# Kernel tuning notes

Hardware: AMD Instinct MI355X
Metric: run time of the kernel (lower is better)

Reference implementation:

```python
import jax, jax.numpy as jnp
import numpy as np

BEAM = 64
RANK = 32
VOCAB = 21128


def setup_inputs() -> dict:
    key = jax.random.key(0)
    k1, k2, k3, k4 = jax.random.split(key, 4)
    B, S, V = 16, 256, VOCAB
    emissions = jax.random.normal(k1, (B, S, V), jnp.float32)
    targets = jax.random.randint(k2, (B, S), 0, V)
    mask = jnp.ones((B, S), dtype=bool)
    E1 = jax.random.normal(k3, (V, RANK), jnp.float32) * 0.02
    E2 = jax.random.normal(k4, (V, RANK), jnp.float32) * 0.02
    return {"emissions": emissions, "targets": targets, "mask": mask, "E1": E1, "E2": E2}


def _crf_llh(emissions, targets, mask, E1, E2, beam=BEAM):
    B, S, V = emissions.shape
    maskf = mask.astype(emissions.dtype)

    # ---- numerator: score of the target path ----
    em = jnp.take_along_axis(emissions, targets[:, :, None], axis=2)[:, :, 0]  # [B,S]
    trans = jnp.sum(E1[targets[:, :-1]] * E2[targets[:, 1:]], axis=2)          # [B,S-1]
    scores = em.at[:, 1:].add(trans)
    numerator = jnp.sum(scores * maskf, axis=1)                                # [B]

    # ---- denominator: beam-approximated normalizer ----
    # force target token into the beam (scatter +inf, then topk indices)
    b_idx = jnp.arange(B)[:, None]
    s_idx = jnp.arange(S)[None, :]
    _em = emissions.at[b_idx, s_idx, targets].set(jnp.inf)
    _, beam_targets = jax.lax.top_k(_em, beam)                                 # [B,S,beam]
    beam_em = jnp.take_along_axis(emissions, beam_targets, axis=2)             # [B,S,beam]

    t1 = E1[beam_targets[:, :-1]]                                              # [B,S-1,beam,rank]
    t2 = E2[beam_targets[:, 1:]]                                               # [B,S-1,beam,rank]
    beam_trans = jnp.einsum('bsir,bsjr->bsij', t1, t2)                         # [B,S-1,beam,beam]

    score0 = beam_em[:, 0]                                                     # [B,beam]

    def step(score, x):
        trans_i, emit_i, m_i = x
        nxt = jax.scipy.special.logsumexp(score[:, :, None] + trans_i, axis=1) + emit_i
        score = jnp.where(m_i[:, None], nxt, score)
        return score, None

    xs = (jnp.swapaxes(beam_trans, 0, 1),          # [S-1,B,beam,beam]
          jnp.swapaxes(beam_em[:, 1:], 0, 1),      # [S-1,B,beam]
          jnp.swapaxes(mask[:, 1:], 0, 1))         # [S-1,B]
    score, _ = jax.lax.scan(step, score0, xs)
    denominator = jax.scipy.special.logsumexp(score, axis=1)                   # [B]

    llh = numerator - denominator
    return jnp.sum(llh)  # reduction='sum'


def reference(emissions, targets, mask, E1, E2):
    return _crf_llh(emissions, targets, mask, E1, E2)
```

## Files before the change

### kernel.cpp

```cpp
#include <hip/hip_runtime.h>
#include <stdint.h>

#define Bn 16
#define Sn 256
#define Vn 21128
#define NV4 5282
#define RANKn 32
#define BEAMn 64
#define HBINS 4096
#define CAPn 512
#define NSEG 16
#define LOG2E 1.44269504088896340736f
#define LN2   0.69314718055994530942f

#define EXP2F(x) __builtin_amdgcn_exp2f(x)
#define LOG2F(x) __builtin_amdgcn_logf(x)

__device__ __forceinline__ unsigned f2o(unsigned b) {
    return (b & 0x80000000u) ? ~b : (b | 0x80000000u);
}
__device__ __forceinline__ float o2f(unsigned u) {
    unsigned b = (u & 0x80000000u) ? (u ^ 0x80000000u) : ~u;
    return __uint_as_float(b);
}
__device__ __forceinline__ float dot4(float4 a, float4 b) {
    return a.x * b.x + a.y * b.y + a.z * b.z + a.w * b.w;
}

__global__ __launch_bounds__(256) void topk_kernel(const float* __restrict__ emis,
                                                   const int* __restrict__ targets,
                                                   const int* __restrict__ mask,
                                                   const float* __restrict__ E1,
                                                   const float* __restrict__ E2,
                                                   int* __restrict__ beam_idx,
                                                   float* __restrict__ beam_val,
                                                   float* __restrict__ out) {
    const int row = blockIdx.x;
    const float* __restrict__ rowp = emis + (size_t)row * Vn;
    const int tgt = targets[row];
    __shared__ unsigned hist[HBINS];
    __shared__ unsigned csum[256];
    __shared__ unsigned cu[CAPn];
    __shared__ int      cix[CAPn];
    __shared__ int      selidx[BEAMn];
    __shared__ float    selval[BEAMn];
    __shared__ unsigned ccount;
    __shared__ int      binstar;
    __shared__ int      chunkc;
    __shared__ int      hastgt;
    __shared__ unsigned wcnt[4];
    const int t = threadIdx.x;
    if (t == 0) { ccount = 0; hastgt = 0; }

    const unsigned THRU = f2o(__float_as_uint(2.5f));
    uint4 vals[21];
    unsigned cntl = 0;
    #pragma unroll
    for (int it = 0; it < 21; ++it) {
        int v4 = t + it * 256;
        if (v4 < NV4) {
            const uint4 raw = ((const uint4*)rowp)[v4];
            uint4 u;
            u.x = f2o(raw.x); u.y = f2o(raw.y); u.z = f2o(raw.z); u.w = f2o(raw.w);
            vals[it] = u;
            cntl += (u.x > THRU) + (u.y > THRU) + (u.z > THRU) + (u.w > THRU);
        }
    }
    for (int off = 32; off; off >>= 1) cntl += __shfl_xor(cntl, off, 64);
    if ((t & 63) == 0) wcnt[t >> 6] = cntl;
    __syncthreads();
    const unsigned C0 = wcnt[0] + wcnt[1] + wcnt[2] + wcnt[3];

    if (C0 >= BEAMn && C0 <= CAPn) {
        #pragma unroll
        for (int it = 0; it < 21; ++it) {
            int v4 = t + it * 256;
            if (v4 < NV4) {
                uint4 u = vals[it];
                int bi = v4 * 4;
                if (u.x > THRU) { unsigned p = atomicAdd(&ccount, 1u); cu[p] = u.x; cix[p] = bi;     }
                if (u.y > THRU) { unsigned p = atomicAdd(&ccount, 1u); cu[p] = u.y; cix[p] = bi + 1; }
                if (u.z > THRU) { unsigned p = atomicAdd(&ccount, 1u); cu[p] = u.z; cix[p] = bi + 2; }
                if (u.w > THRU) { unsigned p = atomicAdd(&ccount, 1u); cu[p] = u.w; cix[p] = bi + 3; }
            }
        }
    } else {
        for (int i = t; i < HBINS; i += 256) hist[i] = 0;
        __syncthreads();
        #pragma unroll
        for (int it = 0; it < 21; ++it) {
            int v4 = t + it * 256;
            if (v4 < NV4) {
                uint4 u = vals[it];
                atomicAdd(&hist[u.x >> 20], 1u);
                atomicAdd(&hist[u.y >> 20], 1u);
                atomicAdd(&hist[u.z >> 20], 1u);
                atomicAdd(&hist[u.w >> 20], 1u);
            }
        }
        __syncthreads();
        unsigned cs = 0;
        #pragma unroll
        for (int i = 0; i < 16; ++i) cs += hist[t * 16 + i];
        csum[t] = cs;
        __syncthreads();
        for (int off = 1; off < 256; off <<= 1) {
            unsigned v = csum[t] + ((t + off < 256) ? csum[t + off] : 0u);
            __syncthreads();
            csum[t] = v;
            __syncthreads();
        }
        if (csum[t] >= BEAMn && (t == 255 || csum[t + 1] < BEAMn)) chunkc = t;
        __syncthreads();
        if (t == 0) {
            int tc = chunkc;
            unsigned acc = (tc == 255) ? 0u : csum[tc + 1];
            int bs = tc * 16;
            for (int b2 = tc * 16 + 15; b2 >= tc * 16; --b2) {
                acc += hist[b2];
                if (acc >= BEAMn) { bs = b2; break; }
            }
            binstar = bs;
        }
        __syncthreads();
        const unsigned bstar = (unsigned)binstar;
        #pragma unroll
        for (int it = 0; it < 21; ++it) {
            int v4 = t + it * 256;
            if (v4 < NV4) {
                uint4 u = vals[it];
                int bi = v4 * 4;
                if ((u.x >> 20) >= bstar) { unsigned p = atomicAdd(&ccount, 1u); if (p < CAPn) { cu[p] = u.x; cix[p] = bi;     } }
                if ((u.y >> 20) >= bstar) { unsigned p = atomicAdd(&ccount, 1u); if (p < CAPn) { cu[p] = u.y; cix[p] = bi + 1; } }
                if ((u.z >> 20) >= bstar) { unsigned p = atomicAdd(&ccount, 1u); if (p < CAPn) { cu[p] = u.z; cix[p] = bi + 2; } }
                if ((u.w >> 20) >= bstar) { unsigned p = atomicAdd(&ccount, 1u); if (p < CAPn) { cu[p] = u.w; cix[p] = bi + 3; } }
            }
        }
    }
    __syncthreads();
    const int C = (int)min(ccount, (unsigned)CAPn);
    for (int p = t; p < C; p += 256) {
        unsigned up = cu[p]; int ip = cix[p];
        int rank = 0;
        for (int q = 0; q < C; ++q) {
            unsigned uq = cu[q];
            rank += (uq > up) || (uq == up && cix[q] < ip);
        }
        if (rank < BEAMn) { selidx[rank] = ip; selval[rank] = o2f(up); }
    }
    __syncthreads();
    if (t < BEAMn && selidx[t] == tgt) hastgt = 1;
    __syncthreads();
    if (t == 0 && !hastgt) { selidx[BEAMn - 1] = tgt; selval[BEAMn - 1] = rowp[tgt]; }
    __syncthreads();
    if (t < BEAMn) {
        beam_idx[(size_t)row * BEAMn + t] = selidx[t];
        beam_val[(size_t)row * BEAMn + t] = selval[t];
    }
    if (t == 0) {
        const int s = row & (Sn - 1);
        float val = 0.f;
        if (mask[row]) {
            float em = rowp[tgt];
            float tr = 0.f;
            if (s > 0) {
                int pv = targets[row - 1];
                const float4* p1 = (const float4*)(E1 + (size_t)pv * RANKn);
                const float4* p2 = (const float4*)(E2 + (size_t)tgt * RANKn);
                #pragma unroll
                for (int r = 0; r < 8; ++r) tr += dot4(p1[r], p2[r]);
            }
            val = em + tr;
        }
        atomicAdd(out, val);
    }
}

#define TPAD 68
__global__ __launch_bounds__(256) void segprod_kernel(const float* __restrict__ E1,
                                                      const float* __restrict__ E2,
                                                      const int* __restrict__ beam_idx,
                                                      const float* __restrict__ beam_val,
                                                      const int* __restrict__ mask,
                                                      float* __restrict__ segP,
                                                      float* __restrict__ segL) {
    const int blk = blockIdx.x;
    const int b = blk >> 4, s = blk & 15;
    const int k0 = s * 16;
    const int nk = min(16, (Sn - 1) - k0);
    const float* __restrict__ bv  = beam_val + (size_t)b * Sn * BEAMn;
    const int* __restrict__ mk   = mask + (size_t)b * Sn;
    const int* __restrict__ bidx = beam_idx + (size_t)b * Sn * BEAMn;
    __shared__ float Qa[64][64], Qb[64][64];
    __shared__ float Mld[64][68];
    __shared__ float e1t[RANKn][TPAD];
    __shared__ float e2t[RANKn][TPAD];
    __shared__ float elog[16][64];
    __shared__ int   mvec[16];
    __shared__ float wmax[4];
    const int t = threadIdx.x;
    const int ti = t & 15, tj = t >> 4;
    const int i0 = ti * 4, j0 = tj * 4;

    for (int x = t; x < 4096; x += 256)
        (&Qa[0][0])[x] = ((x >> 6) == (x & 63)) ? 1.f : 0.f;
    for (int x = t; x < nk * 64; x += 256)
        elog[x >> 6][x & 63] = bv[(size_t)(k0 + (x >> 6) + 1) * BEAMn + (x & 63)] * LOG2E;
    if (t < nk) mvec[t] = mk[k0 + t + 1];
    __syncthreads();

    float (*Qc)[64] = Qa, (*Qn)[64] = Qb;
    float L = 0.f;
    const int srow = t >> 2, sq = t & 3;
    for (int kk = 0; kk < nk; ++kk) {
        const int live = mvec[kk];
        if (live) {
            const int rb = sq * 8;
            int i1 = bidx[(size_t)(k0 + kk) * BEAMn + srow];
            const float4* s1 = (const float4*)(E1 + (size_t)i1 * RANKn) + sq * 2;
            float4 a0 = s1[0], a1 = s1[1];
            int i2 = bidx[(size_t)(k0 + kk + 1) * BEAMn + srow];
            const float4* s2 = (const float4*)(E2 + (size_t)i2 * RANKn) + sq * 2;
            float4 b0 = s2[0], b1 = s2[1];
            e1t[rb + 0][srow] = a0.x; e1t[rb + 1][srow] = a0.y; e1t[rb + 2][srow] = a0.z; e1t[rb + 3][srow] = a0.w;
            e1t[rb + 4][srow] = a1.x; e1t[rb + 5][srow] = a1.y; e1t[rb + 6][srow] = a1.z; e1t[rb + 7][srow] = a1.w;
            e2t[rb + 0][srow] = b0.x; e2t[rb + 1][srow] = b0.y; e2t[rb + 2][srow] = b0.z; e2t[rb + 3][srow] = b0.w;
            e2t[rb + 4][srow] = b1.x; e2t[rb + 5][srow] = b1.y; e2t[rb + 6][srow] = b1.z; e2t[rb + 7][srow] = b1.w;
        }
        __syncthreads();
        if (live) {
            float macc[4][4] = {};
            #pragma unroll
            for (int r = 0; r < RANKn; ++r) {
                float4 a  = *(const float4*)&e1t[r][i0];
                float4 bb = *(const float4*)&e2t[r][j0];
                macc[0][0] += a.x * bb.x; macc[0][1] += a.x * bb.y; macc[0][2] += a.x * bb.z; macc[0][3] += a.x * bb.w;
                macc[1][0] += a.y * bb.x; macc[1][1] += a.y * bb.y; macc[1][2] += a.y * bb.z; macc[1][3] += a.y * bb.w;
                macc[2][0] += a.z * bb.x; macc[2][1] += a.z * bb.y; macc[2][2] += a.z * bb.z; macc[2][3] += a.z * bb.w;
                macc[3][0] += a.w * bb.x; macc[3][1] += a.w * bb.y; macc[3][2] += a.w * bb.z; macc[3][3] += a.w * bb.w;
            }
            const float4 el = *(const float4*)&elog[kk][j0];
            #pragma unroll
            for (int ii = 0; ii < 4; ++ii) {
                float4 o = { EXP2F(macc[ii][0] * LOG2E + el.x), EXP2F(macc[ii][1] * LOG2E + el.y),
                             EXP2F(macc[ii][2] * LOG2E + el.z), EXP2F(macc[ii][3] * LOG2E + el.w) };
                *(float4*)&Mld[i0 + ii][j0] = o;
            }
        }
        __syncthreads();
        float acc[4][4];
        if (live) {
            #pragma unroll
            for (int ii = 0; ii < 4; ++ii)
                #pragma unroll
                for (int jj = 0; jj < 4; ++jj) acc[ii][jj] = 0.f;
            for (int r = 0; r < 64; ++r) {
                float4 a  = *(const float4*)&Qc[r][i0];
                float4 bb = *(const float4*)&Mld[r][j0];
                acc[0][0] += a.x * bb.x; acc[0][1] += a.x * bb.y; acc[0][2] += a.x * bb.z; acc[0][3] += a.x * bb.w;
                acc[1][0] += a.y * bb.x; acc[1][1] += a.y * bb.y; acc[1][2] += a.y * bb.z; acc[1][3] += a.y * bb.w;
                acc[2][0] += a.z * bb.x; acc[2][1] += a.z * bb.y; acc[2][2] += a.z * bb.z; acc[2][3] += a.z * bb.w;
                acc[3][0] += a.w * bb.x; acc[3][1] += a.w * bb.y; acc[3][2] += a.w * bb.z; acc[3][3] += a.w * bb.w;
            }
            float lm = acc[0][0];
            #pragma unroll
            for (int ii = 0; ii < 4; ++ii)
                #pragma unroll
                for (int jj = 0; jj < 4; ++jj) lm = fmaxf(lm, acc[ii][jj]);
            for (int off = 32; off; off >>= 1) lm = fmaxf(lm, __shfl_xor(lm, off, 64));
            if ((t & 63) == 0) wmax[t >> 6] = lm;
        }
        __syncthreads();
        if (live) {
            const float m = fmaxf(fmaxf(wmax[0], wmax[1]), fmaxf(wmax[2], wmax[3]));
            const float inv = 1.f / m;
            #pragma unroll
            for (int jj = 0; jj < 4; ++jj) {
                float4 w = { acc[0][jj] * inv, acc[1][jj] * inv, acc[2][jj] * inv, acc[3][jj] * inv };
                *(float4*)&Qn[j0 + jj][i0] = w;
            }
            L += LOG2F(m);
            float (*tmp)[64] = Qc; Qc = Qn; Qn = tmp;
        }
        __syncthreads();
    }
    float* op = segP + (size_t)blk * 4096;
    for (int x = t; x < 4096; x += 256) op[x] = (&Qc[0][0])[x];
    if (t == 0) segL[blk] = L;
}

__global__ __launch_bounds__(256) void finale_kernel(const float* __restrict__ segP,
                                                     const float* __restrict__ segL,
                                                     const float* __restrict__ beam_val,
                                                     float* __restrict__ out) {
    const int b = blockIdx.x;
    const int t = threadIdx.x;
    const int w = t >> 6, j = t & 63;
    const float* __restrict__ bv = beam_val + (size_t)b * Sn * BEAMn;
    __shared__ float us[BEAMn];
    __shared__ float part[4][BEAMn + 1];
    float sc = bv[j] * LOG2E;
    float mx = sc;
    for (int off = 32; off; off >>= 1) mx = fmaxf(mx, __shfl_xor(mx, off, 64));
    float u = EXP2F(sc - mx);
    float Ltot = mx;
    const float* p0 = segP + ((size_t)b * NSEG) * 4096 + (size_t)j * 64 + w * 16;
    float4 ra0 = ((const float4*)p0)[0], ra1 = ((const float4*)p0)[1],
           ra2 = ((const float4*)p0)[2], ra3 = ((const float4*)p0)[3];
    for (int s2 = 0; s2 < NSEG; ++s2) {
        float4 rb0, rb1, rb2, rb3;
        if (s2 + 1 < NSEG) {
            const float* pn = segP + ((size_t)b * NSEG + s2 + 1) * 4096 + (size_t)j * 64 + w * 16;
            rb0 = ((const float4*)pn)[0]; rb1 = ((const float4*)pn)[1];
            rb2 = ((const float4*)pn)[2]; rb3 = ((const float4*)pn)[3];
        }
        if (w == 0) us[j] = u;
        __syncthreads();
        const float4* uu = (const float4*)&us[w * 16];
        float a2 = dot4(ra0, uu[0]) + dot4(ra1, uu[1]) + dot4(ra2, uu[2]) + dot4(ra3, uu[3]);
        part[w][j] = a2;
        __syncthreads();
        float tot = part[0][j] + part[1][j] + part[2][j] + part[3][j];
        float m = tot;
        for (int off = 32; off; off >>= 1) m = fmaxf(m, __shfl_xor(m, off, 64));
        u = tot / m;
        Ltot += LOG2F(m) + segL[b * NSEG + s2];
        ra0 = rb0; ra1 = rb1; ra2 = rb2; ra3 = rb3;
    }
    if (t < BEAMn) {
        float e = u;
        for (int off = 32; off; off >>= 1) e += __shfl_xor(e, off, 64);
        if (t == 0) atomicAdd(out, -LN2 * (Ltot + LOG2F(e)));
    }
}

extern "C" void kernel_launch(void* const* d_in, const int* in_sizes, int n_in,
                              void* d_out, int out_size, void* d_ws, size_t ws_size,
                              hipStream_t stream) {
    const float* emis    = (const float*)d_in[0];
    const int*   targets = (const int*)d_in[1];
    const int*   mask    = (const int*)d_in[2];
    const float* E1      = (const float*)d_in[3];
    const float* E2      = (const float*)d_in[4];
    float* out = (float*)d_out;
    char* ws = (char*)d_ws;
    int*   beam_idx = (int*)ws;
    float* beam_val = (float*)(ws + (1 << 20));
    float* segP     = (float*)(ws + (2 << 20));
    float* segL     = (float*)(ws + (7 << 20));

    (void)hipMemsetAsync(out, 0, sizeof(float), stream);
    hipLaunchKernelGGL(topk_kernel, dim3(Bn * Sn), dim3(256), 0, stream,
                       emis, targets, mask, E1, E2, beam_idx, beam_val, out);
    hipLaunchKernelGGL(segprod_kernel, dim3(Bn * NSEG), dim3(256), 0, stream,
                       E1, E2, beam_idx, beam_val, mask, segP, segL);
    hipLaunchKernelGGL(finale_kernel, dim3(Bn), dim3(256), 0, stream,
                       segP, segL, beam_val, out);
}
```

Before: 583.0 us.

## Split beam recurrence into 32 shorter segments and normalize once per segment

The sequence is split into 32 segments of 8 steps instead of 16 segments of 16. This doubles the number of segment-product blocks and halves the serial chain each block walks. The per-step max reduction, its extra barrier and the rescale are removed; the segment product is normalized only once at the end. In exchange, unnormalized values grow across 8 steps, which risks overflow, and the finale kernel must combine twice as many segment matrices through a larger workspace.

```diff
diff --git a/kernel.cpp b/kernel.cpp
--- a/kernel.cpp
+++ b/kernel.cpp
@@ -9,7 +9,8 @@
 #define BEAMn 64
 #define HBINS 4096
 #define CAPn 512
-#define NSEG 16
+#define NSEG 32
+#define SEGLEN 8
 #define LOG2E 1.44269504088896340736f
 #define LN2   0.69314718055994530942f
 
@@ -177,17 +178,17 @@
 }
 
 #define TPAD 68
-__global__ __launch_bounds__(256) void segprod_kernel(const float* __restrict__ E1,
-                                                      const float* __restrict__ E2,
-                                                      const int* __restrict__ beam_idx,
-                                                      const float* __restrict__ beam_val,
-                                                      const int* __restrict__ mask,
-                                                      float* __restrict__ segP,
-                                                      float* __restrict__ segL) {
+__global__ __launch_bounds__(256, 2) void segprod_kernel(const float* __restrict__ E1,
+                                                         const float* __restrict__ E2,
+                                                         const int* __restrict__ beam_idx,
+                                                         const float* __restrict__ beam_val,
+                                                         const int* __restrict__ mask,
+                                                         float* __restrict__ segP,
+                                                         float* __restrict__ segL) {
     const int blk = blockIdx.x;
-    const int b = blk >> 4, s = blk & 15;
-    const int k0 = s * 16;
-    const int nk = min(16, (Sn - 1) - k0);
+    const int b = blk >> 5, s = blk & 31;
+    const int k0 = s * SEGLEN;
+    const int nk = min(SEGLEN, (Sn - 1) - k0);
     const float* __restrict__ bv  = beam_val + (size_t)b * Sn * BEAMn;
     const int* __restrict__ mk   = mask + (size_t)b * Sn;
     const int* __restrict__ bidx = beam_idx + (size_t)b * Sn * BEAMn;
@@ -195,9 +196,9 @@
     __shared__ float Mld[64][68];
     __shared__ float e1t[RANKn][TPAD];
     __shared__ float e2t[RANKn][TPAD];
-    __shared__ float elog[16][64];
-    __shared__ int   mvec[16];
-    __shared__ float wmax[4];
+    __shared__ float elog[SEGLEN][64];
+    __shared__ int   mvec[SEGLEN];
+    __shared__ float wred[4];
     const int t = threadIdx.x;
     const int ti = t & 15, tj = t >> 4;
     const int i0 = ti * 4, j0 = tj * 4;
@@ -210,7 +211,6 @@
     __syncthreads();
 
     float (*Qc)[64] = Qa, (*Qn)[64] = Qb;
-    float L = 0.f;
     const int srow = t >> 2, sq = t & 3;
     for (int kk = 0; kk < nk; ++kk) {
         const int live = mvec[kk];
@@ -248,12 +248,8 @@
             }
         }
         __syncthreads();
-        float acc[4][4];
         if (live) {
-            #pragma unroll
-            for (int ii = 0; ii < 4; ++ii)
-                #pragma unroll
-                for (int jj = 0; jj < 4; ++jj) acc[ii][jj] = 0.f;
+            float acc[4][4] = {};
             for (int r = 0; r < 64; ++r) {
                 float4 a  = *(const float4*)&Qc[r][i0];
                 float4 bb = *(const float4*)&Mld[r][j0];
@@ -262,31 +258,25 @@
                 acc[2][0] += a.z * bb.x; acc[2][1] += a.z * bb.y; acc[2][2] += a.z * bb.z; acc[2][3] += a.z * bb.w;
                 acc[3][0] += a.w * bb.x; acc[3][1] += a.w * bb.y; acc[3][2] += a.w * bb.z; acc[3][3] += a.w * bb.w;
             }
-            float lm = acc[0][0];
-            #pragma unroll
-            for (int ii = 0; ii < 4; ++ii)
-                #pragma unroll
-                for (int jj = 0; jj < 4; ++jj) lm = fmaxf(lm, acc[ii][jj]);
-            for (int off = 32; off; off >>= 1) lm = fmaxf(lm, __shfl_xor(lm, off, 64));
-            if ((t & 63) == 0) wmax[t >> 6] = lm;
-        }
-        __syncthreads();
-        if (live) {
-            const float m = fmaxf(fmaxf(wmax[0], wmax[1]), fmaxf(wmax[2], wmax[3]));
-            const float inv = 1.f / m;
             #pragma unroll
             for (int jj = 0; jj < 4; ++jj) {
-                float4 w = { acc[0][jj] * inv, acc[1][jj] * inv, acc[2][jj] * inv, acc[3][jj] * inv };
+                float4 w = { acc[0][jj], acc[1][jj], acc[2][jj], acc[3][jj] };
                 *(float4*)&Qn[j0 + jj][i0] = w;
             }
-            L += LOG2F(m);
             float (*tmp)[64] = Qc; Qc = Qn; Qn = tmp;
         }
         __syncthreads();
     }
+    float lm = 0.f;
+    for (int x = t; x < 4096; x += 256) lm = fmaxf(lm, (&Qc[0][0])[x]);
+    for (int off = 32; off; off >>= 1) lm = fmaxf(lm, __shfl_xor(lm, off, 64));
+    if ((t & 63) == 0) wred[t >> 6] = lm;
+    __syncthreads();
+    const float m = fmaxf(fmaxf(wred[0], wred[1]), fmaxf(wred[2], wred[3]));
+    const float inv = 1.f / m;
     float* op = segP + (size_t)blk * 4096;
-    for (int x = t; x < 4096; x += 256) op[x] = (&Qc[0][0])[x];
-    if (t == 0) segL[blk] = L;
+    for (int x = t; x < 4096; x += 256) op[x] = (&Qc[0][0])[x] * inv;
+    if (t == 0) segL[blk] = LOG2F(m);
 }
 
 __global__ __launch_bounds__(256) void finale_kernel(const float* __restrict__ segP,
@@ -347,7 +337,7 @@
     int*   beam_idx = (int*)ws;
     float* beam_val = (float*)(ws + (1 << 20));
     float* segP     = (float*)(ws + (2 << 20));
-    float* segL     = (float*)(ws + (7 << 20));
+    float* segL     = (float*)(ws + (10 << 20));
 
     (void)hipMemsetAsync(out, 0, sizeof(float), stream);
     hipLaunchKernelGGL(topk_kernel, dim3(Bn * Sn), dim3(256), 0, stream,
```

New measurement: 567.7 us. 1.03x faster.
